# Kernel optimization log

Measured on AMD Instinct MI355X. Metric: run time of the kernel, lower is better.

Reference implementation:

```python
import jax, jax.numpy as jnp
import numpy as np

# DSCNPair config (init_kwargs)
C = 256          # d_model
G = 16           # group
K = 3            # kernel_size
DW = 3           # dw_kernel_size
PAD = 1
STRIDE = 1
DIL = 1
GC = C // G      # group_channels
P = K * K        # sampling points per group
OFFSET_SCALE = 1.0
B, H, W = 8, 64, 64


def _dwconv(x, w, b, pad):
    # depthwise conv: x (N,C,H,W), w (C,1,kh,kw)
    out = jax.lax.conv_general_dilated(
        x, w, (1, 1), [(pad, pad), (pad, pad)],
        dimension_numbers=('NCHW', 'OIHW', 'NCHW'), feature_group_count=x.shape[1])
    return out + b[None, :, None, None]


def _dcn_core(x, offset, mask):
    # x: (N,H,W,C) NHWC; offset: (N,H,W,G*P*2); mask: (N,H,W,G*P) already softmaxed per group
    N, Hh, Ww, _ = x.shape
    xp = jnp.pad(x, ((0, 0), (PAD, PAD), (PAD, PAD), (0, 0)))
    Hp, Wp = Hh + 2 * PAD, Ww + 2 * PAD
    Ho = (Hp - (DIL * (K - 1) + 1)) // STRIDE + 1
    Wo = (Wp - (DIL * (K - 1) + 1)) // STRIDE + 1
    # reference points (normalized by padded spatial size)
    base = (DIL * (K - 1)) // 2 + 0.5
    ref_y = (base + jnp.arange(Ho, dtype=x.dtype) * STRIDE) / Hp
    ref_x = (base + jnp.arange(Wo, dtype=x.dtype) * STRIDE) / Wp
    # dilation grid, kw-major ordering to match torch.meshgrid(lin_w, lin_h) in DCNv3
    pts = -((DIL * (K - 1)) // 2) + jnp.arange(K, dtype=x.dtype) * DIL
    gx = jnp.repeat(pts, K) / Wp
    gy = jnp.tile(pts, K) / Hp
    off = offset.reshape(N, Ho, Wo, G, P, 2) * (OFFSET_SCALE / jnp.array([Wp, Hp], x.dtype))
    loc_x = ref_x[None, None, :, None, None] + OFFSET_SCALE * gx + off[..., 0]  # (N,Ho,Wo,G,P)
    loc_y = ref_y[None, :, None, None, None] + OFFSET_SCALE * gy + off[..., 1]
    # grid_sample(bilinear, padding_mode='zeros', align_corners=False):
    # grid g = 2*loc-1; unnormalized idx = ((g+1)*size - 1)/2 = loc*size - 0.5
    ix = loc_x * Wp - 0.5
    iy = loc_y * Hp - 0.5
    x0 = jnp.floor(ix)
    y0 = jnp.floor(iy)
    xg = xp.reshape(N, Hp, Wp, G, GC)
    n_idx = jnp.arange(N)[:, None, None, None, None]
    g_idx = jnp.arange(G)[None, None, None, :, None]

    def gather(yi, xi):
        valid = ((yi >= 0) & (yi < Hp) & (xi >= 0) & (xi < Wp)).astype(x.dtype)
        yc = jnp.clip(yi, 0, Hp - 1).astype(jnp.int32)
        xc = jnp.clip(xi, 0, Wp - 1).astype(jnp.int32)
        return xg[n_idx, yc, xc, g_idx] * valid[..., None]  # (N,Ho,Wo,G,P,GC)

    wx1 = ix - x0; wx0 = 1.0 - wx1
    wy1 = iy - y0; wy0 = 1.0 - wy1
    out = (gather(y0, x0) * (wy0 * wx0)[..., None]
           + gather(y0, x0 + 1) * (wy0 * wx1)[..., None]
           + gather(y0 + 1, x0) * (wy1 * wx0)[..., None]
           + gather(y0 + 1, x0 + 1) * (wy1 * wx1)[..., None])
    out = (out * mask.reshape(N, Ho, Wo, G, P, 1)).sum(4)   # (N,Ho,Wo,G,GC)
    return out.reshape(N, Ho, Wo, G * GC)


def _forward(x, conv0_w, conv0_b, dw_w, dw_b, ln_g, ln_b, off_w, off_b,
             msk_w, msk_b, in_w, in_b, outp_w, outp_b, pw_w, pw_b):
    u = x
    h = _dwconv(x, conv0_w, conv0_b, 2)             # 5x5 depthwise, pad 2
    inp = jnp.transpose(h, (0, 2, 3, 1))            # NHWC, input to DCNv3
    xproj = inp @ in_w + in_b                       # input_proj
    # dw_conv branch: depthwise conv -> LayerNorm(channels_last) -> GELU
    x1 = _dwconv(jnp.transpose(inp, (0, 3, 1, 2)), dw_w, dw_b, (DW - 1) // 2)
    x1 = jnp.transpose(x1, (0, 2, 3, 1))
    mu = x1.mean(-1, keepdims=True)
    var = jnp.mean((x1 - mu) ** 2, -1, keepdims=True)
    x1 = (x1 - mu) * jax.lax.rsqrt(var + 1e-5) * ln_g + ln_b
    x1 = jax.nn.gelu(x1, approximate=False)
    offset = x1 @ off_w + off_b                     # (B,H,W,G*P*2)
    m = jax.nn.softmax((x1 @ msk_w + msk_b).reshape(B, H, W, G, P), axis=-1)
    m = m.reshape(B, H, W, G * P)
    y = _dcn_core(xproj, offset, m)
    y = y @ outp_w + outp_b                         # output_proj
    attn = jnp.einsum('nhwc,dc->ndhw', y, pw_w) + pw_b[None, :, None, None]  # 1x1 conv
    return u * attn


def setup_inputs() -> dict:
    key = jax.random.key(0)
    ks = jax.random.split(key, 8)
    s = 0.05
    return {
        'x': jax.random.normal(ks[0], (B, C, H, W), jnp.float32),
        'conv0_w': jax.random.normal(ks[1], (C, 1, 5, 5), jnp.float32) * s,
        'conv0_b': jnp.zeros((C,), jnp.float32),
        'dw_w': jax.random.normal(ks[2], (C, 1, DW, DW), jnp.float32) * s,
        'dw_b': jnp.zeros((C,), jnp.float32),
        'ln_g': jnp.ones((C,), jnp.float32),
        'ln_b': jnp.zeros((C,), jnp.float32),
        'off_w': jax.random.normal(ks[3], (C, G * P * 2), jnp.float32) * s,
        'off_b': jnp.zeros((G * P * 2,), jnp.float32),
        'msk_w': jax.random.normal(ks[4], (C, G * P), jnp.float32) * s,
        'msk_b': jnp.zeros((G * P,), jnp.float32),
        'in_w': jax.random.normal(ks[5], (C, C), jnp.float32) * s,
        'in_b': jnp.zeros((C,), jnp.float32),
        'outp_w': jax.random.normal(ks[6], (C, C), jnp.float32) * s,
        'outp_b': jnp.zeros((C,), jnp.float32),
        'pw_w': jax.random.normal(ks[7], (C, C), jnp.float32) * s,
        'pw_b': jnp.zeros((C,), jnp.float32),
    }


def reference(x, conv0_w, conv0_b, dw_w, dw_b, ln_g, ln_b, off_w, off_b,
              msk_w, msk_b, in_w, in_b, outp_w, outp_b, pw_w, pw_b):
    return _forward(x, conv0_w, conv0_b, dw_w, dw_b, ln_g, ln_b, off_w, off_b,
                    msk_w, msk_b, in_w, in_b, outp_w, outp_b, pw_w, pw_b)
```

## Files before the change

kernel.cpp:

```cpp
#include <hip/hip_runtime.h>
#include <hip/hip_bf16.h>
#include <hip/hip_fp16.h>
#include <math.h>

#define BB 8
#define CC 256
#define HH 64
#define WW 64
#define GG 16
#define GCH 16
#define PP 9
#define NPIX (BB*HH*WW)

typedef __attribute__((ext_vector_type(4))) float f32x4;
typedef __bf16 bf16x8 __attribute__((ext_vector_type(8)));

#define GLOAD_LDS16(g, l) __builtin_amdgcn_global_load_lds( \
    (const __attribute__((address_space(1))) unsigned int*)(g), \
    (__attribute__((address_space(3))) unsigned int*)(l), 16, 0, 0)

#define C0PLANE 817
__global__ void conv0_kernel(const float* __restrict__ x, const float* __restrict__ w,
                             const float* __restrict__ b, float* __restrict__ out,
                             __hip_bfloat16* __restrict__ out_bf) {
    __shared__ float sx[16 * C0PLANE];
    int t  = threadIdx.x;
    int st = blockIdx.x;
    int cg = blockIdx.y;
    int n  = blockIdx.z;
    int h0 = st * 8;
    int c0 = cg * 16;

    #pragma unroll
    for (int i = 0; i < 12; ++i) {
        int task = i * 256 + t;
        int lane = task & 15;
        int pair = task >> 4;
        int c    = pair / 12;
        int row  = pair - c * 12;
        int gy   = h0 - 2 + row;
        float4 v = make_float4(0.f, 0.f, 0.f, 0.f);
        if (gy >= 0 && gy < HH)
            v = *(const float4*)(x + (((size_t)(n * CC + c0 + c)) * HH + gy) * WW + lane * 4);
        *(float4*)&sx[c * C0PLANE + row * 68 + 2 + lane * 4] = v;
    }
    if (t < 192) {
        int c = t / 12, row = t - (t / 12) * 12;
        float* p = &sx[c * C0PLANE + row * 68];
        p[0] = 0.f; p[1] = 0.f; p[66] = 0.f; p[67] = 0.f;
    }
    __syncthreads();

    int c = t & 15;
    int s = t >> 4;
    float wreg[25];
    const float* wp = w + (c0 + c) * 25;
    #pragma unroll
    for (int i = 0; i < 25; ++i) wreg[i] = wp[i];
    float bias = b[c0 + c];
    const float* cp = &sx[c * C0PLANE + s * 4];

    float win[5][8];
    #pragma unroll
    for (int rr = 0; rr < 4; ++rr)
        #pragma unroll
        for (int j = 0; j < 8; ++j) win[rr][j] = cp[rr * 68 + j];

    #pragma unroll
    for (int r = 0; r < 8; ++r) {
        #pragma unroll
        for (int j = 0; j < 8; ++j) win[(r + 4) % 5][j] = cp[(r + 4) * 68 + j];
        float a0 = bias, a1 = bias, a2 = bias, a3 = bias;
        #pragma unroll
        for (int dy = 0; dy < 5; ++dy) {
            const float* wr = &wreg[dy * 5];
            const float* wd = win[(r + dy) % 5];
            #pragma unroll
            for (int dx = 0; dx < 5; ++dx) {
                float wv = wr[dx];
                a0 += wd[0 + dx] * wv;
                a1 += wd[1 + dx] * wv;
                a2 += wd[2 + dx] * wv;
                a3 += wd[3 + dx] * wv;
            }
        }
        size_t pixb = ((size_t)n * 4096 + (h0 + r) * 64 + s * 4) << 8;
        out[pixb + c0 + c]         = a0;
        out[pixb + 256 + c0 + c]   = a1;
        out[pixb + 512 + c0 + c]   = a2;
        out[pixb + 768 + c0 + c]   = a3;
        out_bf[pixb + c0 + c]       = __float2bfloat16(a0);
        out_bf[pixb + 256 + c0 + c] = __float2bfloat16(a1);
        out_bf[pixb + 512 + c0 + c] = __float2bfloat16(a2);
        out_bf[pixb + 768 + c0 + c] = __float2bfloat16(a3);
    }
}

__global__ void dwln_kernel(const float* __restrict__ inp, const float* __restrict__ dww,
                            const float* __restrict__ dwb, const float* __restrict__ lng,
                            const float* __restrict__ lnb, __hip_bfloat16* __restrict__ x1) {
    __shared__ float sx[3 * 10 * 256];
    __shared__ float ls1[8][4], ls2[8][4];
    int t  = threadIdx.x;
    int x0 = blockIdx.x * 8;
    int h  = blockIdx.y;
    int n  = blockIdx.z;

    #pragma unroll
    for (int i = 0; i < 8; ++i) {
        int task = i * 256 + t;
        if (task < 1920) {
            int c4  = task & 63;
            int rem = task >> 6;
            int r   = rem / 10;
            int xx  = rem - r * 10;
            int gy = h + r - 1, gx = x0 + xx - 1;
            float4 v = make_float4(0.f, 0.f, 0.f, 0.f);
            if (gy >= 0 && gy < HH && gx >= 0 && gx < WW)
                v = *(const float4*)(inp + (((size_t)(n * HH + gy)) * WW + gx) * CC + c4 * 4);
            *(float4*)&sx[(r * 10 + xx) * 256 + c4 * 4] = v;
        }
    }
    __syncthreads();

    int c = t;
    float wr[9];
    #pragma unroll
    for (int i = 0; i < 9; ++i) wr[i] = dww[c * 9 + i];
    float bias = dwb[c];
    float a[8];
    #pragma unroll
    for (int px = 0; px < 8; ++px) {
        float acc = bias;
        #pragma unroll
        for (int dy = 0; dy < 3; ++dy)
            #pragma unroll
            for (int dx = 0; dx < 3; ++dx)
                acc += sx[(dy * 10 + px + dx) * 256 + c] * wr[dy * 3 + dx];
        a[px] = acc;
    }

    int wid = t >> 6, lane = t & 63;
    #pragma unroll
    for (int px = 0; px < 8; ++px) {
        float s1 = a[px], s2 = a[px] * a[px];
        #pragma unroll
        for (int o = 1; o < 64; o <<= 1) {
            s1 += __shfl_xor(s1, o);
            s2 += __shfl_xor(s2, o);
        }
        if (lane == 0) { ls1[px][wid] = s1; ls2[px][wid] = s2; }
    }
    __syncthreads();

    float gam = lng[c], bet = lnb[c];
    #pragma unroll
    for (int px = 0; px < 8; ++px) {
        float t1 = ls1[px][0] + ls1[px][1] + ls1[px][2] + ls1[px][3];
        float t2 = ls2[px][0] + ls2[px][1] + ls2[px][2] + ls2[px][3];
        float mu  = t1 * (1.0f/256.0f);
        float var = t2 * (1.0f/256.0f) - mu * mu;
        float rr  = rsqrtf(var + 1e-5f);
        float v = (a[px] - mu) * rr * gam + bet;
        float g = 0.5f * v * (1.0f + erff(v * 0.70710678118654752440f));
        x1[(((size_t)(n * HH + h)) * WW + x0 + px) * CC + c] = __float2bfloat16(g);
    }
}

__global__ void wcvt_t_kernel(const float* __restrict__ W, __hip_bfloat16* __restrict__ Bt, int N) {
    int idx = blockIdx.x * 256 + threadIdx.x;
    int n = idx >> 8, k = idx & 255;
    float v = (n < N) ? W[k * N + n] : 0.0f;
    Bt[idx] = __float2bfloat16(v);
}
__global__ void wcvt_n_kernel(const float* __restrict__ W, __hip_bfloat16* __restrict__ Bt) {
    int idx = blockIdx.x * 256 + threadIdx.x;
    Bt[idx] = __float2bfloat16(W[idx]);
}

__device__ __forceinline__ void stage_tile(const __hip_bfloat16* __restrict__ A,
                                           const __hip_bfloat16* __restrict__ Bt,
                                           __bf16* As, __bf16* Bs,
                                           int bm, int bn, int k0, int w, int l) {
    #pragma unroll
    for (int i = 0; i < 4; ++i) {
        int q = w*256 + i*64 + l;
        int row = q >> 3, sk = q & 7;
        const __hip_bfloat16* g = A + (((size_t)(bm + row)) << 8) + k0 + sk*8;
        GLOAD_LDS16(g, As + (w*256 + i*64)*8);
    }
    #pragma unroll
    for (int i = 0; i < 2; ++i) {
        int q = w*128 + i*64 + l;
        int row = q >> 3, sk = q & 7;
        const __hip_bfloat16* g = Bt + (((size_t)(bn + row)) << 8) + k0 + sk*8;
        GLOAD_LDS16(g, Bs + (w*128 + i*64)*8);
    }
}

template <int OUT_BF16, int NBOUND>
__global__ void mgemm_kernel(const __hip_bfloat16* __restrict__ A,
                             const __hip_bfloat16* __restrict__ Bt,
                             const float* __restrict__ bias,
                             void* __restrict__ Cout, int N, int ldc) {
    __shared__ __bf16 smem[24576];
    int tid = threadIdx.x;
    int w = tid >> 6, l = tid & 63;
    int bn = blockIdx.x * 64;
    int bm = blockIdx.y * 128;
    __bf16* Asb[2] = { smem,        smem + 12288 };
    __bf16* Bsb[2] = { smem + 8192, smem + 20480 };
    f32x4 acc[2][4];
    #pragma unroll
    for (int m = 0; m < 2; ++m)
        #pragma unroll
        for (int n = 0; n < 4; ++n)
            acc[m][n] = (f32x4){0.f, 0.f, 0.f, 0.f};

    stage_tile(A, Bt, Asb[0], Bsb[0], bm, bn, 0, w, l);
    __syncthreads();
    int lr = l & 15, kg = l >> 4;
    #pragma unroll
    for (int t = 0; t < 4; ++t) {
        int cur = t & 1;
        if (t < 3) stage_tile(A, Bt, Asb[cur^1], Bsb[cur^1], bm, bn, (t+1)*64, w, l);
        const __bf16* Ab = Asb[cur];
        const __bf16* Bb = Bsb[cur];
        bf16x8 af[2][2], bfr[4][2];
        #pragma unroll
        for (int m = 0; m < 2; ++m)
            #pragma unroll
            for (int u = 0; u < 2; ++u)
                af[m][u] = *(const bf16x8*)&Ab[(w*32 + m*16 + lr)*64 + u*32 + kg*8];
        #pragma unroll
        for (int n = 0; n < 4; ++n)
            #pragma unroll
            for (int u = 0; u < 2; ++u)
                bfr[n][u] = *(const bf16x8*)&Bb[(n*16 + lr)*64 + u*32 + kg*8];
        #pragma unroll
        for (int u = 0; u < 2; ++u)
            #pragma unroll
            for (int m = 0; m < 2; ++m)
                #pragma unroll
                for (int n = 0; n < 4; ++n)
                    acc[m][n] = __builtin_amdgcn_mfma_f32_16x16x32_bf16(af[m][u], bfr[n][u], acc[m][n], 0, 0, 0);
        __syncthreads();
    }
    int orow = bm + w*32 + kg*4;
    #pragma unroll
    for (int n = 0; n < 4; ++n) {
        int ccol = bn + n*16 + lr;
        if (NBOUND && ccol >= N) continue;
        float bv = bias[ccol];
        #pragma unroll
        for (int m = 0; m < 2; ++m) {
            #pragma unroll
            for (int j = 0; j < 4; ++j) {
                size_t o = (size_t)(orow + m*16 + j) * ldc + ccol;
                float v = acc[m][n][j] + bv;
                if (OUT_BF16) ((__hip_bfloat16*)Cout)[o] = __float2bfloat16(v);
                else          ((float*)Cout)[o] = v;
            }
        }
    }
}

__device__ __forceinline__ void bfu2(unsigned a, float& lo, float& hi) {
    union { unsigned u; float f; } t0, t1;
    t0.u = a << 16; t1.u = a & 0xffff0000u;
    lo = t0.f; hi = t1.f;
}

__global__ void dcn_kernel(const __hip_bfloat16* __restrict__ xproj,
                           const float* __restrict__ off,
                           const float* __restrict__ mlog,
                           __hip_bfloat16* __restrict__ y) {
    __shared__ uint2 wLds[1152];
    __shared__ int   oLds[1152];
    int pix0 = blockIdx.x * 8;
    int t = threadIdx.x;

    if (t < 128) {
        int px = t >> 4;
        int g  = t & 15;
        int pix = pix0 + px;
        int wo = pix & 63, ho = (pix >> 6) & 63;
        const float* mb = mlog + (size_t)pix * 144 + g * 9;
        float lg[9];
        float mx = -1e30f;
        #pragma unroll
        for (int p = 0; p < 9; ++p) { lg[p] = mb[p]; mx = fmaxf(mx, lg[p]); }
        float se = 0.f;
        #pragma unroll
        for (int p = 0; p < 9; ++p) { lg[p] = __expf(lg[p] - mx); se += lg[p]; }
        float rs = 1.0f / se;
        const float* ob = off + (size_t)pix * 288 + g * 18;
        #pragma unroll
        for (int p = 0; p < 9; ++p) {
            float2 o2 = *(const float2*)(ob + p * 2);
            float m = lg[p] * rs;
            int dx = p / 3 - 1;
            int dy = p - (p / 3) * 3 - 1;
            float fx = (float)(wo + dx) + o2.x;
            float fy = (float)(ho + dy) + o2.y;
            float x0f = floorf(fx), y0f = floorf(fy);
            int x0 = (int)x0f, y0 = (int)y0f;
            int x1 = x0 + 1, y1 = y0 + 1;
            float wx1 = fx - x0f, wx0 = 1.0f - wx1;
            float wy1 = fy - y0f, wy0 = 1.0f - wy1;
            float vx0 = (x0 >= 0 && x0 < WW) ? 1.0f : 0.0f;
            float vx1 = (x1 >= 0 && x1 < WW) ? 1.0f : 0.0f;
            float vy0 = (y0 >= 0 && y0 < HH) ? 1.0f : 0.0f;
            float vy1 = (y1 >= 0 && y1 < HH) ? 1.0f : 0.0f;
            int x0c = min(max(x0, 0), WW - 1), x1c = min(max(x1, 0), WW - 1);
            int y0c = min(max(y0, 0), HH - 1), y1c = min(max(y1, 0), HH - 1);
            int tau = px * 144 + g * 9 + p;
            union { __half2 h2; unsigned u; } pa, pb;
            pa.h2 = __floats2half2_rn(m * wy0 * wx0 * vy0 * vx0,
                                      m * wy0 * wx1 * vy0 * vx1);
            pb.h2 = __floats2half2_rn(m * wy1 * wx0 * vy1 * vx0,
                                      m * wy1 * wx1 * vy1 * vx1);
            wLds[tau] = make_uint2(pa.u, pb.u);
            oLds[tau] = (y0c * WW + x0c) | ((x1c - x0c) << 12) | ((y1c - y0c) << 13);
        }
    }
    __syncthreads();

    int px = t >> 5;
    int l  = t & 31;
    int g  = l >> 1;
    int ch = g * 16 + (l & 1) * 8;
    int pix = pix0 + px;
    int n = pix >> 12;
    const __hip_bfloat16* xb = xproj + ((size_t)n << 20) + ch;
    float a0=0,a1=0,a2=0,a3=0,a4=0,a5=0,a6=0,a7=0;
    const uint2* wp = &wLds[px * 144 + g * 9];
    const int*   op = &oLds[px * 144 + g * 9];
    #pragma unroll
    for (int p = 0; p < 9; ++p) {
        uint2 pw = wp[p];
        union { unsigned u; __half2 h2; } ua, ub;
        ua.u = pw.x; ub.u = pw.y;
        float2 fA = __half22float2(ua.h2);
        float2 fB = __half22float2(ub.h2);
        float w00 = fA.x, w01 = fA.y, w10 = fB.x, w11 = fB.y;
        int pk = op[p];
        int base = (pk & 4095) << 8;
        int ddx  = ((pk >> 12) & 1) << 8;
        int ddy  = ((pk >> 13) & 1) << 14;
        {
            uint4 u = *(const uint4*)(xb + base);
            float b0,b1,b2,b3,b4,b5,b6,b7;
            bfu2(u.x,b0,b1); bfu2(u.y,b2,b3); bfu2(u.z,b4,b5); bfu2(u.w,b6,b7);
            a0 += w00*b0; a1 += w00*b1; a2 += w00*b2; a3 += w00*b3;
            a4 += w00*b4; a5 += w00*b5; a6 += w00*b6; a7 += w00*b7;
        }
        {
            uint4 u = *(const uint4*)(xb + base + ddx);
            float b0,b1,b2,b3,b4,b5,b6,b7;
            bfu2(u.x,b0,b1); bfu2(u.y,b2,b3); bfu2(u.z,b4,b5); bfu2(u.w,b6,b7);
            a0 += w01*b0; a1 += w01*b1; a2 += w01*b2; a3 += w01*b3;
            a4 += w01*b4; a5 += w01*b5; a6 += w01*b6; a7 += w01*b7;
        }
        {
            uint4 u = *(const uint4*)(xb + base + ddy);
            float b0,b1,b2,b3,b4,b5,b6,b7;
            bfu2(u.x,b0,b1); bfu2(u.y,b2,b3); bfu2(u.z,b4,b5); bfu2(u.w,b6,b7);
            a0 += w10*b0; a1 += w10*b1; a2 += w10*b2; a3 += w10*b3;
            a4 += w10*b4; a5 += w10*b5; a6 += w10*b6; a7 += w10*b7;
        }
        {
            uint4 u = *(const uint4*)(xb + base + ddy + ddx);
            float b0,b1,b2,b3,b4,b5,b6,b7;
            bfu2(u.x,b0,b1); bfu2(u.y,b2,b3); bfu2(u.z,b4,b5); bfu2(u.w,b6,b7);
            a0 += w11*b0; a1 += w11*b1; a2 += w11*b2; a3 += w11*b3;
            a4 += w11*b4; a5 += w11*b5; a6 += w11*b6; a7 += w11*b7;
        }
    }
    union { __hip_bfloat16 h[8]; uint4 u; } ov;
    ov.h[0]=__float2bfloat16(a0); ov.h[1]=__float2bfloat16(a1);
    ov.h[2]=__float2bfloat16(a2); ov.h[3]=__float2bfloat16(a3);
    ov.h[4]=__float2bfloat16(a4); ov.h[5]=__float2bfloat16(a5);
    ov.h[6]=__float2bfloat16(a6); ov.h[7]=__float2bfloat16(a7);
    *(uint4*)(y + (size_t)pix * CC + ch) = ov.u;
}

__global__ void finmul_kernel(const float* __restrict__ x, const float* __restrict__ attn,
                              float* __restrict__ out) {
    __shared__ float t[16][17];
    int pix0 = blockIdx.x * 16;
    int d0   = blockIdx.y * 16;
    int li = threadIdx.x & 15;
    int lj = threadIdx.x >> 4;
    t[lj][li] = attn[(size_t)(pix0 + lj)*CC + d0 + li];
    __syncthreads();
    int pix = pix0 + li;
    int wo = pix & 63;
    int ho = (pix >> 6) & 63;
    int n  = pix >> 12;
    int d = d0 + lj;
    size_t oidx = (((size_t)n*CC + d)*HH + ho)*WW + wo;
    out[oidx] = x[oidx] * t[li][lj];
}

extern "C" void kernel_launch(void* const* d_in, const int* in_sizes, int n_in,
                              void* d_out, int out_size, void* d_ws, size_t ws_size,
                              hipStream_t stream) {
    const float* x      = (const float*)d_in[0];
    const float* conv0w = (const float*)d_in[1];
    const float* conv0b = (const float*)d_in[2];
    const float* dww    = (const float*)d_in[3];
    const float* dwb    = (const float*)d_in[4];
    const float* lng    = (const float*)d_in[5];
    const float* lnb    = (const float*)d_in[6];
    const float* offw   = (const float*)d_in[7];
    const float* offb   = (const float*)d_in[8];
    const float* mskw   = (const float*)d_in[9];
    const float* mskb   = (const float*)d_in[10];
    const float* inw    = (const float*)d_in[11];
    const float* inb    = (const float*)d_in[12];
    const float* outpw  = (const float*)d_in[13];
    const float* outpb  = (const float*)d_in[14];
    const float* pww    = (const float*)d_in[15];
    const float* pwb    = (const float*)d_in[16];

    float* ws   = (float*)d_ws;
    float* off  = ws;
    float* msk  = ws + 9437184;
    float* inpf = ws + 14155776;
    float* attn = inpf;
    __hip_bfloat16* bfb    = (__hip_bfloat16*)(ws + 22544384);
    __hip_bfloat16* inp_bf = bfb;
    __hip_bfloat16* y_bf   = inp_bf;
    __hip_bfloat16* x1_bf  = bfb + 8388608;
    __hip_bfloat16* xpj_bf = x1_bf;
    __hip_bfloat16* z_bf   = x1_bf;
    __hip_bfloat16* bt_in   = bfb + 16777216;
    __hip_bfloat16* bt_off  = bt_in  + 65536;
    __hip_bfloat16* bt_msk  = bt_off + 81920;
    __hip_bfloat16* bt_outp = bt_msk + 49152;
    __hip_bfloat16* bt_pw   = bt_outp + 65536;
    float* out = (float*)d_out;

    wcvt_t_kernel<<<256, 256, 0, stream>>>(inw,   bt_in,   256);
    wcvt_t_kernel<<<320, 256, 0, stream>>>(offw,  bt_off,  288);
    wcvt_t_kernel<<<192, 256, 0, stream>>>(mskw,  bt_msk,  144);
    wcvt_t_kernel<<<256, 256, 0, stream>>>(outpw, bt_outp, 256);
    wcvt_n_kernel<<<256, 256, 0, stream>>>(pww,   bt_pw);

    conv0_kernel<<<dim3(8, 16, BB), 256, 0, stream>>>(x, conv0w, conv0b, inpf, inp_bf);
    dwln_kernel<<<dim3(8, 64, BB), 256, 0, stream>>>(inpf, dww, dwb, lng, lnb, x1_bf);
    mgemm_kernel<0,1><<<dim3(5, 256), 256, 0, stream>>>(x1_bf, bt_off, offb, off, 288, 288);
    mgemm_kernel<0,1><<<dim3(3, 256), 256, 0, stream>>>(x1_bf, bt_msk, mskb, msk, 144, 144);
    mgemm_kernel<1,0><<<dim3(4, 256), 256, 0, stream>>>(inp_bf, bt_in, inb, xpj_bf, 256, 256);
    dcn_kernel<<<NPIX/8, 256, 0, stream>>>(xpj_bf, off, msk, y_bf);
    mgemm_kernel<1,0><<<dim3(4, 256), 256, 0, stream>>>(y_bf, bt_outp, outpb, z_bf, 256, 256);
    mgemm_kernel<0,0><<<dim3(4, 256), 256, 0, stream>>>(z_bf, bt_pw, pwb, attn, 256, 256);
    finmul_kernel<<<dim3(NPIX/16, 16), 256, 0, stream>>>(x, attn, out);
}
```

Measured before the change: 204.8 us.

## Fold output and pointwise projections into one GEMM, store intermediates as bf16

```diff
diff --git a/kernel.cpp b/kernel.cpp
--- a/kernel.cpp
+++ b/kernel.cpp
@@ -19,9 +19,15 @@
     (const __attribute__((address_space(1))) unsigned int*)(g), \
     (__attribute__((address_space(3))) unsigned int*)(l), 16, 0, 0)
 
+__device__ __forceinline__ void bfu2(unsigned a, float& lo, float& hi) {
+    union { unsigned u; float f; } t0, t1;
+    t0.u = a << 16; t1.u = a & 0xffff0000u;
+    lo = t0.f; hi = t1.f;
+}
+
 #define C0PLANE 817
 __global__ void conv0_kernel(const float* __restrict__ x, const float* __restrict__ w,
-                             const float* __restrict__ b, float* __restrict__ out,
+                             const float* __restrict__ b,
                              __hip_bfloat16* __restrict__ out_bf) {
     __shared__ float sx[16 * C0PLANE];
     int t  = threadIdx.x;
@@ -85,10 +91,6 @@
             }
         }
         size_t pixb = ((size_t)n * 4096 + (h0 + r) * 64 + s * 4) << 8;
-        out[pixb + c0 + c]         = a0;
-        out[pixb + 256 + c0 + c]   = a1;
-        out[pixb + 512 + c0 + c]   = a2;
-        out[pixb + 768 + c0 + c]   = a3;
         out_bf[pixb + c0 + c]       = __float2bfloat16(a0);
         out_bf[pixb + 256 + c0 + c] = __float2bfloat16(a1);
         out_bf[pixb + 512 + c0 + c] = __float2bfloat16(a2);
@@ -96,7 +98,7 @@
     }
 }
 
-__global__ void dwln_kernel(const float* __restrict__ inp, const float* __restrict__ dww,
+__global__ void dwln_kernel(const __hip_bfloat16* __restrict__ inp, const float* __restrict__ dww,
                             const float* __restrict__ dwb, const float* __restrict__ lng,
                             const float* __restrict__ lnb, __hip_bfloat16* __restrict__ x1) {
     __shared__ float sx[3 * 10 * 256];
@@ -107,18 +109,22 @@
     int n  = blockIdx.z;
 
     #pragma unroll
-    for (int i = 0; i < 8; ++i) {
+    for (int i = 0; i < 4; ++i) {
         int task = i * 256 + t;
-        if (task < 1920) {
-            int c4  = task & 63;
-            int rem = task >> 6;
+        if (task < 960) {
+            int c8  = task & 31;
+            int rem = task >> 5;
             int r   = rem / 10;
             int xx  = rem - r * 10;
             int gy = h + r - 1, gx = x0 + xx - 1;
-            float4 v = make_float4(0.f, 0.f, 0.f, 0.f);
-            if (gy >= 0 && gy < HH && gx >= 0 && gx < WW)
-                v = *(const float4*)(inp + (((size_t)(n * HH + gy)) * WW + gx) * CC + c4 * 4);
-            *(float4*)&sx[(r * 10 + xx) * 256 + c4 * 4] = v;
+            float4 A = make_float4(0.f,0.f,0.f,0.f), B = make_float4(0.f,0.f,0.f,0.f);
+            if (gy >= 0 && gy < HH && gx >= 0 && gx < WW) {
+                uint4 u = *(const uint4*)(inp + (((size_t)(n * HH + gy)) * WW + gx) * CC + c8 * 8);
+                bfu2(u.x, A.x, A.y); bfu2(u.y, A.z, A.w);
+                bfu2(u.z, B.x, B.y); bfu2(u.w, B.z, B.w);
+            }
+            *(float4*)&sx[(r * 10 + xx) * 256 + c8 * 8]     = A;
+            *(float4*)&sx[(r * 10 + xx) * 256 + c8 * 8 + 4] = B;
         }
     }
     __syncthreads();
@@ -173,9 +179,26 @@
     float v = (n < N) ? W[k * N + n] : 0.0f;
     Bt[idx] = __float2bfloat16(v);
 }
-__global__ void wcvt_n_kernel(const float* __restrict__ W, __hip_bfloat16* __restrict__ Bt) {
-    int idx = blockIdx.x * 256 + threadIdx.x;
-    Bt[idx] = __float2bfloat16(W[idx]);
+__global__ void wcomb_kernel(const float* __restrict__ outpw, const float* __restrict__ pww,
+                             __hip_bfloat16* __restrict__ Wc) {
+    __shared__ float pd[256];
+    int d = blockIdx.x, k = threadIdx.x;
+    pd[k] = pww[d * 256 + k];
+    __syncthreads();
+    const float* ow = outpw + k * 256;
+    float s = 0.0f;
+    #pragma unroll 8
+    for (int c = 0; c < 256; ++c) s += ow[c] * pd[c];
+    Wc[d * 256 + k] = __float2bfloat16(s);
+}
+__global__ void bcomb_kernel(const float* __restrict__ outpb, const float* __restrict__ pww,
+                             const float* __restrict__ pwb, float* __restrict__ bc) {
+    int d = threadIdx.x;
+    const float* pr = pww + d * 256;
+    float s = pwb[d];
+    #pragma unroll 8
+    for (int c = 0; c < 256; ++c) s += outpb[c] * pr[c];
+    bc[d] = s;
 }
 
 __device__ __forceinline__ void stage_tile(const __hip_bfloat16* __restrict__ A,
@@ -265,15 +288,9 @@
     }
 }
 
-__device__ __forceinline__ void bfu2(unsigned a, float& lo, float& hi) {
-    union { unsigned u; float f; } t0, t1;
-    t0.u = a << 16; t1.u = a & 0xffff0000u;
-    lo = t0.f; hi = t1.f;
-}
-
 __global__ void dcn_kernel(const __hip_bfloat16* __restrict__ xproj,
-                           const float* __restrict__ off,
-                           const float* __restrict__ mlog,
+                           const __hip_bfloat16* __restrict__ off,
+                           const __hip_bfloat16* __restrict__ mlog,
                            __hip_bfloat16* __restrict__ y) {
     __shared__ uint2 wLds[1152];
     __shared__ int   oLds[1152];
@@ -285,24 +302,25 @@
         int g  = t & 15;
         int pix = pix0 + px;
         int wo = pix & 63, ho = (pix >> 6) & 63;
-        const float* mb = mlog + (size_t)pix * 144 + g * 9;
+        const __hip_bfloat16* mb = mlog + (size_t)pix * 144 + g * 9;
         float lg[9];
         float mx = -1e30f;
         #pragma unroll
-        for (int p = 0; p < 9; ++p) { lg[p] = mb[p]; mx = fmaxf(mx, lg[p]); }
+        for (int p = 0; p < 9; ++p) { lg[p] = __bfloat162float(mb[p]); mx = fmaxf(mx, lg[p]); }
         float se = 0.f;
         #pragma unroll
         for (int p = 0; p < 9; ++p) { lg[p] = __expf(lg[p] - mx); se += lg[p]; }
         float rs = 1.0f / se;
-        const float* ob = off + (size_t)pix * 288 + g * 18;
+        const unsigned* ob = (const unsigned*)(off + (size_t)pix * 288 + g * 18);
         #pragma unroll
         for (int p = 0; p < 9; ++p) {
-            float2 o2 = *(const float2*)(ob + p * 2);
+            float ox, oy;
+            bfu2(ob[p], ox, oy);
             float m = lg[p] * rs;
             int dx = p / 3 - 1;
             int dy = p - (p / 3) * 3 - 1;
-            float fx = (float)(wo + dx) + o2.x;
-            float fy = (float)(ho + dy) + o2.y;
+            float fx = (float)(wo + dx) + ox;
+            float fy = (float)(ho + dy) + oy;
             float x0f = floorf(fx), y0f = floorf(fy);
             int x0 = (int)x0f, y0 = (int)y0f;
             int x1 = x0 + 1, y1 = y0 + 1;
@@ -385,14 +403,14 @@
     *(uint4*)(y + (size_t)pix * CC + ch) = ov.u;
 }
 
-__global__ void finmul_kernel(const float* __restrict__ x, const float* __restrict__ attn,
+__global__ void finmul_kernel(const float* __restrict__ x, const __hip_bfloat16* __restrict__ attn,
                               float* __restrict__ out) {
     __shared__ float t[16][17];
     int pix0 = blockIdx.x * 16;
     int d0   = blockIdx.y * 16;
     int li = threadIdx.x & 15;
     int lj = threadIdx.x >> 4;
-    t[lj][li] = attn[(size_t)(pix0 + lj)*CC + d0 + li];
+    t[lj][li] = __bfloat162float(attn[(size_t)(pix0 + lj)*CC + d0 + li]);
     __syncthreads();
     int pix = pix0 + li;
     int wo = pix & 63;
@@ -424,37 +442,33 @@
     const float* pww    = (const float*)d_in[15];
     const float* pwb    = (const float*)d_in[16];
 
-    float* ws   = (float*)d_ws;
-    float* off  = ws;
-    float* msk  = ws + 9437184;
-    float* inpf = ws + 14155776;
-    float* attn = inpf;
-    __hip_bfloat16* bfb    = (__hip_bfloat16*)(ws + 22544384);
-    __hip_bfloat16* inp_bf = bfb;
-    __hip_bfloat16* y_bf   = inp_bf;
-    __hip_bfloat16* x1_bf  = bfb + 8388608;
-    __hip_bfloat16* xpj_bf = x1_bf;
-    __hip_bfloat16* z_bf   = x1_bf;
-    __hip_bfloat16* bt_in   = bfb + 16777216;
+    __hip_bfloat16* bfb = (__hip_bfloat16*)d_ws;
+    __hip_bfloat16* inp_bf  = bfb;
+    __hip_bfloat16* y_bf    = inp_bf;
+    __hip_bfloat16* x1_bf   = bfb + 8388608;
+    __hip_bfloat16* xpj_bf  = x1_bf;
+    __hip_bfloat16* attn_bf = x1_bf;
+    __hip_bfloat16* off_bf  = bfb + 16777216;
+    __hip_bfloat16* msk_bf  = bfb + 26214400;
+    __hip_bfloat16* bt_in   = bfb + 30932992;
     __hip_bfloat16* bt_off  = bt_in  + 65536;
     __hip_bfloat16* bt_msk  = bt_off + 81920;
-    __hip_bfloat16* bt_outp = bt_msk + 49152;
-    __hip_bfloat16* bt_pw   = bt_outp + 65536;
+    __hip_bfloat16* bt_wc   = bt_msk + 49152;
+    float* bcomb = (float*)(bt_wc + 65536);
     float* out = (float*)d_out;
 
-    wcvt_t_kernel<<<256, 256, 0, stream>>>(inw,   bt_in,   256);
-    wcvt_t_kernel<<<320, 256, 0, stream>>>(offw,  bt_off,  288);
-    wcvt_t_kernel<<<192, 256, 0, stream>>>(mskw,  bt_msk,  144);
-    wcvt_t_kernel<<<256, 256, 0, stream>>>(outpw, bt_outp, 256);
-    wcvt_n_kernel<<<256, 256, 0, stream>>>(pww,   bt_pw);
-
-    conv0_kernel<<<dim3(8, 16, BB), 256, 0, stream>>>(x, conv0w, conv0b, inpf, inp_bf);
-    dwln_kernel<<<dim3(8, 64, BB), 256, 0, stream>>>(inpf, dww, dwb, lng, lnb, x1_bf);
-    mgemm_kernel<0,1><<<dim3(5, 256), 256, 0, stream>>>(x1_bf, bt_off, offb, off, 288, 288);
-    mgemm_kernel<0,1><<<dim3(3, 256), 256, 0, stream>>>(x1_bf, bt_msk, mskb, msk, 144, 144);
+    wcvt_t_kernel<<<256, 256, 0, stream>>>(inw,  bt_in,  256);
+    wcvt_t_kernel<<<320, 256, 0, stream>>>(offw, bt_off, 288);
+    wcvt_t_kernel<<<192, 256, 0, stream>>>(mskw, bt_msk, 144);
+    wcomb_kernel<<<256, 256, 0, stream>>>(outpw, pww, bt_wc);
+    bcomb_kernel<<<1, 256, 0, stream>>>(outpb, pww, pwb, bcomb);
+
+    conv0_kernel<<<dim3(8, 16, BB), 256, 0, stream>>>(x, conv0w, conv0b, inp_bf);
+    dwln_kernel<<<dim3(8, 64, BB), 256, 0, stream>>>(inp_bf, dww, dwb, lng, lnb, x1_bf);
+    mgemm_kernel<1,1><<<dim3(5, 256), 256, 0, stream>>>(x1_bf, bt_off, offb, off_bf, 288, 288);
+    mgemm_kernel<1,1><<<dim3(3, 256), 256, 0, stream>>>(x1_bf, bt_msk, mskb, msk_bf, 144, 144);
     mgemm_kernel<1,0><<<dim3(4, 256), 256, 0, stream>>>(inp_bf, bt_in, inb, xpj_bf, 256, 256);
-    dcn_kernel<<<NPIX/8, 256, 0, stream>>>(xpj_bf, off, msk, y_bf);
-    mgemm_kernel<1,0><<<dim3(4, 256), 256, 0, stream>>>(y_bf, bt_outp, outpb, z_bf, 256, 256);
-    mgemm_kernel<0,0><<<dim3(4, 256), 256, 0, stream>>>(z_bf, bt_pw, pwb, attn, 256, 256);
-    finmul_kernel<<<dim3(NPIX/16, 16), 256, 0, stream>>>(x, attn, out);
-}
+    dcn_kernel<<<NPIX/8, 256, 0, stream>>>(xpj_bf, off_bf, msk_bf, y_bf);
+    mgemm_kernel<1,0><<<dim3(4, 256), 256, 0, stream>>>(y_bf, bt_wc, bcomb, attn_bf, 256, 256);
+    finmul_kernel<<<dim3(NPIX/16, 16), 256, 0, stream>>>(x, attn_bf, out);
+}
```

Result: faster. 192.3 us (-6.1%).
